# Kernel optimization log

Measured on AMD Instinct MI355X. Metric: run time of the kernel, lower is better.

## Reference

```python
import jax, jax.numpy as jnp
import numpy as np

B, N = 1024, 32768


def setup_inputs() -> dict:
    key = jax.random.key(0)
    k1, k2 = jax.random.split(key)
    outputs = jax.random.normal(k1, (B, N), dtype=jnp.float32)
    # reference pulse rates in Hz, inside the pulse band (40/60, 250/60) Hz
    u = jax.random.uniform(k2, (B, 1), dtype=jnp.float32)
    targets = 0.8 + 3.1 * u
    return {"outputs": outputs, "targets": targets, "Fs": 20}


def reference(outputs, targets, Fs):
    n = outputs.shape[-1]
    nf = n // 2 + 1
    f = jnp.linspace(0.0, Fs / 2.0, nf, dtype=jnp.float32)  # (F,)
    min_idx = jnp.argmin(jnp.abs(f - 40.0 / 60.0))
    max_idx = jnp.argmin(jnp.abs(f - 250.0 / 60.0))

    # torch.rfft(..., normalized=True) == orthonormal rFFT; P1 = |X|^2
    X = jnp.fft.rfft(outputs, norm="ortho")  # (B, F) complex
    P1 = X.real ** 2 + X.imag ** 2  # (B, F)

    # per-sample nearest freq bin to the reference rate
    ref_idx = jnp.argmin(jnp.abs(f[None, :] - targets), axis=1)  # (B,)

    idx = jnp.arange(nf)[None, :]  # (1, F)
    r = ref_idx[:, None]  # (B, 1)
    # slices [min_idx : ref_idx-1] and [ref_idx+2 : max_idx]
    mask = ((idx >= min_idx) & (idx < r - 1)) | ((idx >= r + 2) & (idx < max_idx))
    denom = (max_idx - min_idx - 3).astype(jnp.float32)
    other_avg = jnp.sum(P1 * mask, axis=1) / denom  # (B,)

    pulse_amp = jnp.take_along_axis(P1, ref_idx[:, None], axis=1)[:, 0]  # (B,)
    losses = -10.0 * jnp.log10(pulse_amp / other_avg)
    return jnp.mean(losses)
```

## Files before the change

kernel.cpp:

```cpp
#include <hip/hip_runtime.h>
#include <hip/hip_fp16.h>
#include <math.h>

#define BROWS 1024
#define NPTS  32768
#define MPTS  16384
#define NTHR  512
#define MIN_IDX 1092
#define MAX_IDX 6827
#define DENOMF  5732.0f


#define LD 132

typedef _Float16 h8 __attribute__((ext_vector_type(8)));
typedef float    f4 __attribute__((ext_vector_type(4)));

#define MFMA(a, b, c) __builtin_amdgcn_mfma_f32_16x16x32_f16((a), (b), (c), 0, 0, 0)

#define ANG128 (-0.04908738521234052f)
#define ANG16K (-3.834951969714103e-4f)
#define ANG32K (-1.9174759848570515e-4f)


struct Frag { h8 r, i; };

__device__ inline Frag load_frag(const __half2* __restrict__ base) {
    const float4* p = reinterpret_cast<const float4*>(base);
    union { float4 f; _Float16 h[8]; } a, b;
    a.f = p[0]; b.f = p[1];
    Frag fr;
    fr.r = (h8){a.h[0], a.h[2], a.h[4], a.h[6], b.h[0], b.h[2], b.h[4], b.h[6]};
    fr.i = (h8){a.h[1], a.h[3], a.h[5], a.h[7], b.h[1], b.h[3], b.h[5], b.h[7]};
    return fr;
}

__device__ inline void make_F(int row, int kbase, h8& fr, h8& fi) {
    #pragma unroll
    for (int j = 0; j < 8; ++j) {
        int e = (row * (kbase + j)) & 127;
        float ang = ANG128 * (float)e;
        float s, c;
        __sincosf(ang, &s, &c);
        fr[j] = (_Float16)c;
        fi[j] = (_Float16)s;
    }
}

__device__ inline float bin_pow(const __half2* __restrict__ C, int k) {
    float2 a  = __half22float2(C[(k >> 7) * LD + (k & 127)]);
    int p = MPTS - k;
    float2 bz = __half22float2(C[(p >> 7) * LD + (p & 127)]);
    float bx = bz.x, by = -bz.y;
    float ex = 0.5f * (a.x + bx), ey = 0.5f * (a.y + by);
    float dx = a.x - bx,          dy = a.y - by;
    float ox = 0.5f * dy,         oy = -0.5f * dx;
    float ang = ANG32K * (float)k;
    float c, sn;
    __sincosf(ang, &sn, &c);
    float Xx = ex + ox * c - oy * sn;
    float Xy = ey + ox * sn + oy * c;
    return (Xx * Xx + Xy * Xy) * (1.0f / (float)NPTS);
}

__global__ __launch_bounds__(NTHR, 4) void snr_row_kernel(
        const float* __restrict__ outs,
        const float* __restrict__ targets,
        float* __restrict__ row_loss) {
    __shared__ __align__(16) __half2 bufA[128 * LD];
    __shared__ float red[NTHR / 64];

    const int b    = blockIdx.x;
    const int tid  = threadIdx.x;
    const int lane = tid & 63;
    const int w    = tid >> 6;
    const int r15  = lane & 15;
    const int g    = lane >> 4;
    const float2* row = reinterpret_cast<const float2*>(outs + (size_t)b * NPTS);

    #pragma unroll 1
    for (int it = 0; it < 4; ++it) {
        int T  = tid + NTHR * it;
        int n2 = T & 127;
        int jb = T >> 7;
        __half2 t[8];
        #pragma unroll
        for (int i = 0; i < 8; ++i) {
            float2 v = row[(8 * jb + i) * 128 + n2];
            t[i] = __floats2half2_rn(v.x, v.y);
        }
        float4* dst = reinterpret_cast<float4*>(&bufA[n2 * LD + 8 * jb]);
        dst[0] = *reinterpret_cast<const float4*>(&t[0]);
        dst[1] = *reinterpret_cast<const float4*>(&t[4]);
    }

    h8 fr[4], fi[4];
    #pragma unroll
    for (int kc = 0; kc < 4; ++kc)
        make_F(16 * w + r15, 32 * kc + 8 * g, fr[kc], fi[kc]);
    __syncthreads();

    __half2 bm[8][4];
    #pragma unroll
    for (int n0 = 0; n0 < 8; ++n0) {
        f4 accr = {0.f, 0.f, 0.f, 0.f}, acci = {0.f, 0.f, 0.f, 0.f};
        #pragma unroll
        for (int kc = 0; kc < 4; ++kc) {
            Frag z = load_frag(&bufA[(16 * n0 + r15) * LD + 32 * kc + 8 * g]);
            h8 fin = -fi[kc];
            accr = MFMA(fr[kc], z.r, accr);
            accr = MFMA(fin,    z.i, accr);
            acci = MFMA(fr[kc], z.i, acci);
            acci = MFMA(fi[kc], z.r, acci);
        }
        #pragma unroll
        for (int v = 0; v < 4; ++v) {
            int k1 = 16 * w + 4 * g + v;
            int n2 = 16 * n0 + r15;
            int e  = (k1 * n2) & 16383;
            float s, c;
            __sincosf(ANG16K * (float)e, &s, &c);
            bm[n0][v] = __floats2half2_rn(accr[v] * c - acci[v] * s,
                                          accr[v] * s + acci[v] * c);
        }
    }
    __syncthreads();

    #pragma unroll
    for (int n0 = 0; n0 < 8; ++n0)
        #pragma unroll
        for (int v = 0; v < 4; ++v)
            bufA[(16 * w + 4 * g + v) * LD + 16 * n0 + r15] = bm[n0][v];
    __syncthreads();

    __half2 ct[8][4];
    #pragma unroll
    for (int m0 = 0; m0 < 8; ++m0) {
        f4 accr = {0.f, 0.f, 0.f, 0.f}, acci = {0.f, 0.f, 0.f, 0.f};
        #pragma unroll
        for (int kc = 0; kc < 4; ++kc) {
            Frag a = load_frag(&bufA[(16 * m0 + r15) * LD + 32 * kc + 8 * g]);
            h8 ain = -a.i;
            accr = MFMA(a.r, fr[kc], accr);
            accr = MFMA(ain, fi[kc], accr);
            acci = MFMA(a.r, fi[kc], acci);
            acci = MFMA(a.i, fr[kc], acci);
        }
        #pragma unroll
        for (int v = 0; v < 4; ++v)
            ct[m0][v] = __floats2half2_rn(accr[v], acci[v]);
    }
    __syncthreads();

    #pragma unroll
    for (int m0 = 0; m0 < 8; ++m0)
        #pragma unroll
        for (int v = 0; v < 4; ++v)
            bufA[(16 * w + r15) * LD + 16 * m0 + 4 * g + v] = ct[m0][v];
    __syncthreads();

    float local = 0.0f;
    for (int k = MIN_IDX + tid; k < MAX_IDX; k += NTHR)
        local += bin_pow(bufA, k);

    for (int off = 32; off; off >>= 1) local += __shfl_down(local, off);
    if (lane == 0) red[w] = local;
    __syncthreads();

    if (tid == 0) {
        float S = 0.0f;
        #pragma unroll
        for (int q = 0; q < NTHR / 64; ++q) S += red[q];

        float tgt = targets[b];
        double kd = (double)tgt * (16384.0 / 10.0);
        int k0 = (int)kd;
        const float stepf = 10.0f / 16384.0f;
        float f0 = (float)k0 * stepf;
        float f1 = (float)(k0 + 1) * stepf;
        float d0 = fabsf(f0 - tgt);
        float d1 = fabsf(f1 - tgt);
        int rr = (d0 <= d1) ? k0 : (k0 + 1);

        float pm1 = bin_pow(bufA, rr - 1);
        float p0  = bin_pow(bufA, rr);
        float pp1 = bin_pow(bufA, rr + 1);
        float other_avg = (S - pm1 - p0 - pp1) * (1.0f / DENOMF);
        row_loss[b] = -10.0f * log10f(p0 / other_avg);
    }
}

__global__ __launch_bounds__(256) void snr_reduce_kernel(
        const float* __restrict__ row_loss, float* __restrict__ out) {
    __shared__ float red[4];
    float s = 0.0f;
    for (int i = threadIdx.x; i < BROWS; i += 256) s += row_loss[i];
    for (int off = 32; off; off >>= 1) s += __shfl_down(s, off);
    if ((threadIdx.x & 63) == 0) red[threadIdx.x >> 6] = s;
    __syncthreads();
    if (threadIdx.x == 0)
        out[0] = (red[0] + red[1] + red[2] + red[3]) * (1.0f / (float)BROWS);
}

extern "C" void kernel_launch(void* const* d_in, const int* in_sizes, int n_in,
                              void* d_out, int out_size, void* d_ws, size_t ws_size,
                              hipStream_t stream) {
    const float* outs    = (const float*)d_in[0];
    const float* targets = (const float*)d_in[1];
    float* ws  = (float*)d_ws;
    float* out = (float*)d_out;

    snr_row_kernel<<<BROWS, NTHR, 0, stream>>>(outs, targets, ws);
    snr_reduce_kernel<<<1, 256, 0, stream>>>(ws, out);
}
```

Baseline: 60.95 us.

## Process two rows per block and fuse final reduction via last-block atomic counter

Each block now handles two rows in sequence, reusing the twiddle fragments computed once in registers, and the grid shrinks to half as many blocks. The separate reduction kernel is removed: each block bumps a global atomic counter and the last block to finish sums the per-row losses and writes the mean. This aims to save a kernel launch and the repeated twiddle setup, but it adds a memset launch and serial per-block work, and halving the grid may lower parallelism across CUs.

After: 123.6 us. 103% more time.

```diff
diff --git a/kernel.cpp b/kernel.cpp
--- a/kernel.cpp
+++ b/kernel.cpp
@@ -6,6 +6,7 @@
 #define NPTS  32768
 #define MPTS  16384
 #define NTHR  512
+#define RPB   2
 #define MIN_IDX 1092
 #define MAX_IDX 6827
 #define DENOMF  5732.0f
@@ -66,140 +67,156 @@
 __global__ __launch_bounds__(NTHR, 4) void snr_row_kernel(
         const float* __restrict__ outs,
         const float* __restrict__ targets,
-        float* __restrict__ row_loss) {
+        float* __restrict__ row_loss,
+        unsigned int* __restrict__ counter,
+        float* __restrict__ out) {
     __shared__ __align__(16) __half2 bufA[128 * LD];
     __shared__ float red[NTHR / 64];
-
-    const int b    = blockIdx.x;
+    __shared__ unsigned int lastv;
+
     const int tid  = threadIdx.x;
     const int lane = tid & 63;
     const int w    = tid >> 6;
     const int r15  = lane & 15;
     const int g    = lane >> 4;
-    const float2* row = reinterpret_cast<const float2*>(outs + (size_t)b * NPTS);
-
-    #pragma unroll 1
-    for (int it = 0; it < 4; ++it) {
-        int T  = tid + NTHR * it;
-        int n2 = T & 127;
-        int jb = T >> 7;
-        __half2 t[8];
-        #pragma unroll
-        for (int i = 0; i < 8; ++i) {
-            float2 v = row[(8 * jb + i) * 128 + n2];
-            t[i] = __floats2half2_rn(v.x, v.y);
-        }
-        float4* dst = reinterpret_cast<float4*>(&bufA[n2 * LD + 8 * jb]);
-        dst[0] = *reinterpret_cast<const float4*>(&t[0]);
-        dst[1] = *reinterpret_cast<const float4*>(&t[4]);
-    }
 
     h8 fr[4], fi[4];
     #pragma unroll
     for (int kc = 0; kc < 4; ++kc)
         make_F(16 * w + r15, 32 * kc + 8 * g, fr[kc], fi[kc]);
+
+    #pragma unroll 1
+    for (int rr = 0; rr < RPB; ++rr) {
+        const int b = RPB * blockIdx.x + rr;
+        const float2* row = reinterpret_cast<const float2*>(outs + (size_t)b * NPTS);
+        if (rr) __syncthreads();
+
+        #pragma unroll 1
+        for (int it = 0; it < 4; ++it) {
+            int T  = tid + NTHR * it;
+            int n2 = T & 127;
+            int jb = T >> 7;
+            __half2 t[8];
+            #pragma unroll
+            for (int i = 0; i < 8; ++i) {
+                float2 v = row[(8 * jb + i) * 128 + n2];
+                t[i] = __floats2half2_rn(v.x, v.y);
+            }
+            float4* dst = reinterpret_cast<float4*>(&bufA[n2 * LD + 8 * jb]);
+            dst[0] = *reinterpret_cast<const float4*>(&t[0]);
+            dst[1] = *reinterpret_cast<const float4*>(&t[4]);
+        }
+        __syncthreads();
+
+        __half2 bm[8][4];
+        #pragma unroll
+        for (int n0 = 0; n0 < 8; ++n0) {
+            f4 accr = {0.f, 0.f, 0.f, 0.f}, acci = {0.f, 0.f, 0.f, 0.f};
+            #pragma unroll
+            for (int kc = 0; kc < 4; ++kc) {
+                Frag z = load_frag(&bufA[(16 * n0 + r15) * LD + 32 * kc + 8 * g]);
+                h8 fin = -fi[kc];
+                accr = MFMA(fr[kc], z.r, accr);
+                accr = MFMA(fin,    z.i, accr);
+                acci = MFMA(fr[kc], z.i, acci);
+                acci = MFMA(fi[kc], z.r, acci);
+            }
+            #pragma unroll
+            for (int v = 0; v < 4; ++v) {
+                int k1 = 16 * w + 4 * g + v;
+                int n2 = 16 * n0 + r15;
+                int e  = (k1 * n2) & 16383;
+                float s, c;
+                __sincosf(ANG16K * (float)e, &s, &c);
+                bm[n0][v] = __floats2half2_rn(accr[v] * c - acci[v] * s,
+                                              accr[v] * s + acci[v] * c);
+            }
+        }
+        __syncthreads();
+
+        #pragma unroll
+        for (int n0 = 0; n0 < 8; ++n0)
+            #pragma unroll
+            for (int v = 0; v < 4; ++v)
+                bufA[(16 * w + 4 * g + v) * LD + 16 * n0 + r15] = bm[n0][v];
+        __syncthreads();
+
+        __half2 ct[8][4];
+        #pragma unroll
+        for (int m0 = 0; m0 < 8; ++m0) {
+            f4 accr = {0.f, 0.f, 0.f, 0.f}, acci = {0.f, 0.f, 0.f, 0.f};
+            #pragma unroll
+            for (int kc = 0; kc < 4; ++kc) {
+                Frag a = load_frag(&bufA[(16 * m0 + r15) * LD + 32 * kc + 8 * g]);
+                h8 ain = -a.i;
+                accr = MFMA(a.r, fr[kc], accr);
+                accr = MFMA(ain, fi[kc], accr);
+                acci = MFMA(a.r, fi[kc], acci);
+                acci = MFMA(a.i, fr[kc], acci);
+            }
+            #pragma unroll
+            for (int v = 0; v < 4; ++v)
+                ct[m0][v] = __floats2half2_rn(accr[v], acci[v]);
+        }
+        __syncthreads();
+
+        #pragma unroll
+        for (int m0 = 0; m0 < 8; ++m0)
+            #pragma unroll
+            for (int v = 0; v < 4; ++v)
+                bufA[(16 * w + r15) * LD + 16 * m0 + 4 * g + v] = ct[m0][v];
+        __syncthreads();
+
+        float local = 0.0f;
+        #pragma unroll 2
+        for (int k = MIN_IDX + tid; k < MAX_IDX; k += NTHR)
+            local += bin_pow(bufA, k);
+
+        for (int off = 32; off; off >>= 1) local += __shfl_down(local, off);
+        if (lane == 0) red[w] = local;
+        __syncthreads();
+
+        if (tid == 0) {
+            float S = 0.0f;
+            #pragma unroll
+            for (int q = 0; q < NTHR / 64; ++q) S += red[q];
+
+            float tgt = targets[b];
+            double kd = (double)tgt * (16384.0 / 10.0);
+            int k0 = (int)kd;
+            const float stepf = 10.0f / 16384.0f;
+            float f0 = (float)k0 * stepf;
+            float f1 = (float)(k0 + 1) * stepf;
+            float d0 = fabsf(f0 - tgt);
+            float d1 = fabsf(f1 - tgt);
+            int ri = (d0 <= d1) ? k0 : (k0 + 1);
+
+            float pm1 = bin_pow(bufA, ri - 1);
+            float p0  = bin_pow(bufA, ri);
+            float pp1 = bin_pow(bufA, ri + 1);
+            float other_avg = (S - pm1 - p0 - pp1) * (1.0f / DENOMF);
+            atomicExch(&row_loss[b], -10.0f * log10f(p0 / other_avg));
+        }
+    }
+
     __syncthreads();
-
-    __half2 bm[8][4];
-    #pragma unroll
-    for (int n0 = 0; n0 < 8; ++n0) {
-        f4 accr = {0.f, 0.f, 0.f, 0.f}, acci = {0.f, 0.f, 0.f, 0.f};
-        #pragma unroll
-        for (int kc = 0; kc < 4; ++kc) {
-            Frag z = load_frag(&bufA[(16 * n0 + r15) * LD + 32 * kc + 8 * g]);
-            h8 fin = -fi[kc];
-            accr = MFMA(fr[kc], z.r, accr);
-            accr = MFMA(fin,    z.i, accr);
-            acci = MFMA(fr[kc], z.i, acci);
-            acci = MFMA(fi[kc], z.r, acci);
-        }
-        #pragma unroll
-        for (int v = 0; v < 4; ++v) {
-            int k1 = 16 * w + 4 * g + v;
-            int n2 = 16 * n0 + r15;
-            int e  = (k1 * n2) & 16383;
-            float s, c;
-            __sincosf(ANG16K * (float)e, &s, &c);
-            bm[n0][v] = __floats2half2_rn(accr[v] * c - acci[v] * s,
-                                          accr[v] * s + acci[v] * c);
+    if (tid == 0) lastv = atomicAdd(counter, 1u);
+    __syncthreads();
+    if (lastv == (BROWS / RPB) - 1) {
+        float s = 0.0f;
+        #pragma unroll
+        for (int i = 0; i < BROWS / NTHR; ++i)
+            s += atomicAdd(&row_loss[tid + i * NTHR], 0.0f);
+        for (int off = 32; off; off >>= 1) s += __shfl_down(s, off);
+        if (lane == 0) red[w] = s;
+        __syncthreads();
+        if (tid == 0) {
+            float S = 0.0f;
+            #pragma unroll
+            for (int q = 0; q < NTHR / 64; ++q) S += red[q];
+            out[0] = S * (1.0f / (float)BROWS);
         }
     }
-    __syncthreads();
-
-    #pragma unroll
-    for (int n0 = 0; n0 < 8; ++n0)
-        #pragma unroll
-        for (int v = 0; v < 4; ++v)
-            bufA[(16 * w + 4 * g + v) * LD + 16 * n0 + r15] = bm[n0][v];
-    __syncthreads();
-
-    __half2 ct[8][4];
-    #pragma unroll
-    for (int m0 = 0; m0 < 8; ++m0) {
-        f4 accr = {0.f, 0.f, 0.f, 0.f}, acci = {0.f, 0.f, 0.f, 0.f};
-        #pragma unroll
-        for (int kc = 0; kc < 4; ++kc) {
-            Frag a = load_frag(&bufA[(16 * m0 + r15) * LD + 32 * kc + 8 * g]);
-            h8 ain = -a.i;
-            accr = MFMA(a.r, fr[kc], accr);
-            accr = MFMA(ain, fi[kc], accr);
-            acci = MFMA(a.r, fi[kc], acci);
-            acci = MFMA(a.i, fr[kc], acci);
-        }
-        #pragma unroll
-        for (int v = 0; v < 4; ++v)
-            ct[m0][v] = __floats2half2_rn(accr[v], acci[v]);
-    }
-    __syncthreads();
-
-    #pragma unroll
-    for (int m0 = 0; m0 < 8; ++m0)
-        #pragma unroll
-        for (int v = 0; v < 4; ++v)
-            bufA[(16 * w + r15) * LD + 16 * m0 + 4 * g + v] = ct[m0][v];
-    __syncthreads();
-
-    float local = 0.0f;
-    for (int k = MIN_IDX + tid; k < MAX_IDX; k += NTHR)
-        local += bin_pow(bufA, k);
-
-    for (int off = 32; off; off >>= 1) local += __shfl_down(local, off);
-    if (lane == 0) red[w] = local;
-    __syncthreads();
-
-    if (tid == 0) {
-        float S = 0.0f;
-        #pragma unroll
-        for (int q = 0; q < NTHR / 64; ++q) S += red[q];
-
-        float tgt = targets[b];
-        double kd = (double)tgt * (16384.0 / 10.0);
-        int k0 = (int)kd;
-        const float stepf = 10.0f / 16384.0f;
-        float f0 = (float)k0 * stepf;
-        float f1 = (float)(k0 + 1) * stepf;
-        float d0 = fabsf(f0 - tgt);
-        float d1 = fabsf(f1 - tgt);
-        int rr = (d0 <= d1) ? k0 : (k0 + 1);
-
-        float pm1 = bin_pow(bufA, rr - 1);
-        float p0  = bin_pow(bufA, rr);
-        float pp1 = bin_pow(bufA, rr + 1);
-        float other_avg = (S - pm1 - p0 - pp1) * (1.0f / DENOMF);
-        row_loss[b] = -10.0f * log10f(p0 / other_avg);
-    }
-}
-
-__global__ __launch_bounds__(256) void snr_reduce_kernel(
-        const float* __restrict__ row_loss, float* __restrict__ out) {
-    __shared__ float red[4];
-    float s = 0.0f;
-    for (int i = threadIdx.x; i < BROWS; i += 256) s += row_loss[i];
-    for (int off = 32; off; off >>= 1) s += __shfl_down(s, off);
-    if ((threadIdx.x & 63) == 0) red[threadIdx.x >> 6] = s;
-    __syncthreads();
-    if (threadIdx.x == 0)
-        out[0] = (red[0] + red[1] + red[2] + red[3]) * (1.0f / (float)BROWS);
 }
 
 extern "C" void kernel_launch(void* const* d_in, const int* in_sizes, int n_in,
@@ -207,9 +224,11 @@
                               hipStream_t stream) {
     const float* outs    = (const float*)d_in[0];
     const float* targets = (const float*)d_in[1];
-    float* ws  = (float*)d_ws;
+    float* row_loss = (float*)d_ws;
+    unsigned int* counter = (unsigned int*)((char*)d_ws + 4096);
     float* out = (float*)d_out;
 
-    snr_row_kernel<<<BROWS, NTHR, 0, stream>>>(outs, targets, ws);
-    snr_reduce_kernel<<<1, 256, 0, stream>>>(ws, out);
-}
+    hipMemsetAsync(counter, 0, sizeof(unsigned int), stream);
+    snr_row_kernel<<<BROWS / RPB, NTHR, 0, stream>>>(outs, targets, row_loss,
+                                                     counter, out);
+}
```
